# Optimization experiments

Measured on AMD Instinct MI355X. Metric: run time of the kernel, lower is better.

Reference implementation:

```python
import jax, jax.numpy as jnp
import numpy as np

# Mamba hyperparameters (match init_kwargs)
D_MODEL = 1024
D_STATE = 16
D_CONV = 4
EXPAND = 2
D_INNER = EXPAND * D_MODEL          # 2048
DT_RANK = D_MODEL // 16             # 64 (ceil(d_model/16))
B, L = 2, 2048
LN_EPS = 1e-5


def setup_inputs() -> dict:
    key = jax.random.key(0)
    ks = jax.random.split(key, 8)
    s = lambda k, shape, scale=0.02: jax.random.normal(k, shape, jnp.float32) * scale
    x = jax.random.normal(ks[0], (B, L, D_MODEL), jnp.float32)
    W_in = s(ks[1], (2 * D_INNER, D_MODEL))                 # in_proj (no bias)
    W_conv = s(ks[2], (D_INNER, 1, D_CONV), 0.1)            # depthwise conv1d weight
    b_conv = jnp.zeros((D_INNER,), jnp.float32)
    W_xproj = s(ks[3], (DT_RANK + 2 * D_STATE, D_INNER))    # x_proj (no bias)
    W_dt = s(ks[4], (D_INNER, DT_RANK), 0.1)                # dt_proj weight
    b_dt = s(ks[5], (D_INNER,), 0.5)                        # dt_proj bias
    # A initialized as -exp(A_log) with A_log = log(1..d_state), as in mamba_ssm
    A_log = jnp.log(jnp.broadcast_to(
        jnp.arange(1, D_STATE + 1, dtype=jnp.float32), (D_INNER, D_STATE)))
    D_skip = jnp.ones((D_INNER,), jnp.float32)
    W_out = s(ks[6], (D_MODEL, D_INNER))                    # out_proj (no bias)
    gamma = jnp.ones((D_MODEL,), jnp.float32)
    beta = jnp.zeros((D_MODEL,), jnp.float32)
    return dict(x=x, W_in=W_in, W_conv=W_conv, b_conv=b_conv, W_xproj=W_xproj,
                W_dt=W_dt, b_dt=b_dt, A_log=A_log, D_skip=D_skip, W_out=W_out,
                gamma=gamma, beta=beta)


def _mamba(x, W_in, W_conv, b_conv, W_xproj, W_dt, b_dt, A_log, D_skip, W_out):
    # in_proj -> split into x branch and gate z branch, each [B, L, d_inner]
    xz = jnp.einsum('bld,ed->ble', x, W_in)
    xin, z = jnp.split(xz, 2, axis=-1)

    # causal depthwise conv1d over time, then SiLU
    xc = jnp.swapaxes(xin, 1, 2)                            # [B, d_inner, L]
    xc = jnp.pad(xc, ((0, 0), (0, 0), (D_CONV - 1, 0)))
    xc = jax.lax.conv_general_dilated(
        xc, W_conv, window_strides=(1,), padding='VALID',
        dimension_numbers=('NCH', 'OIH', 'NCH'), feature_group_count=D_INNER)
    xc = xc + b_conv[None, :, None]
    u = jax.nn.silu(jnp.swapaxes(xc, 1, 2))                 # [B, L, d_inner]

    # input-dependent dt, B, C
    xdb = jnp.einsum('ble,fe->blf', u, W_xproj)
    dt, Bm, Cm = jnp.split(xdb, [DT_RANK, DT_RANK + D_STATE], axis=-1)
    delta = jax.nn.softplus(jnp.einsum('blr,er->ble', dt, W_dt) + b_dt)  # [B,L,E]
    A = -jnp.exp(A_log)                                     # [E, N]

    def step(h, inp):
        d_t, B_t, C_t, u_t = inp                            # [B,E],[B,N],[B,N],[B,E]
        dA = jnp.exp(d_t[..., None] * A)                    # [B, E, N]
        dBu = d_t[..., None] * B_t[:, None, :] * u_t[..., None]
        h = dA * h + dBu                                    # [B, E, N]
        y = jnp.einsum('ben,bn->be', h, C_t)
        return h, y

    h0 = jnp.zeros((B, D_INNER, D_STATE), x.dtype)
    xs = (jnp.swapaxes(delta, 0, 1), jnp.swapaxes(Bm, 0, 1),
          jnp.swapaxes(Cm, 0, 1), jnp.swapaxes(u, 0, 1))
    _, ys = jax.lax.scan(step, h0, xs)                      # ys: [L, B, E]
    y = jnp.swapaxes(ys, 0, 1) + u * D_skip
    y = y * jax.nn.silu(z)                                  # gated
    return jnp.einsum('ble,de->bld', y, W_out)


def reference(x, W_in, W_conv, b_conv, W_xproj, W_dt, b_dt, A_log, D_skip,
              W_out, gamma, beta):
    out = x + _mamba(x, W_in, W_conv, b_conv, W_xproj, W_dt, b_dt, A_log,
                     D_skip, W_out)
    mu = jnp.mean(out, axis=-1, keepdims=True)
    var = jnp.mean(jnp.square(out - mu), axis=-1, keepdims=True)
    return (out - mu) * jax.lax.rsqrt(var + LN_EPS) * gamma + beta
```

## Files before the change

### kernel.cpp

```cpp
#include <hip/hip_runtime.h>
#include <cstdint>
#include <cstddef>

#define D_MODEL   1024
#define D_STATE   16
#define D_CONV    4
#define D_INNER   2048
#define DT_RANK   64
#define NBATCH    2
#define SEQ       2048
#define NTOK      (NBATCH*SEQ)
#define LN_EPSF   1e-5f
#define NCHUNK    64
#define TCHUNK    32
#define KSPLIT    8

typedef unsigned short u16;
typedef __bf16 bf16x8 __attribute__((ext_vector_type(8)));
typedef float  f32x4  __attribute__((ext_vector_type(4)));

__device__ __forceinline__ u16 f2bf(float f) {
  unsigned u = __float_as_uint(f);
  u += 0x7fffu + ((u >> 16) & 1u);
  return (u16)(u >> 16);
}
__device__ __forceinline__ float bf2f(u16 v) {
  return __uint_as_float(((unsigned)v) << 16);
}
__device__ __forceinline__ void unpack8(uint4 v, float* f) {
  f[0] = __uint_as_float(v.x << 16); f[1] = __uint_as_float(v.x & 0xffff0000u);
  f[2] = __uint_as_float(v.y << 16); f[3] = __uint_as_float(v.y & 0xffff0000u);
  f[4] = __uint_as_float(v.z << 16); f[5] = __uint_as_float(v.z & 0xffff0000u);
  f[6] = __uint_as_float(v.w << 16); f[7] = __uint_as_float(v.w & 0xffff0000u);
}

__device__ __forceinline__ void async16(const u16* g, u16* l) {
  __builtin_amdgcn_global_load_lds(
      (const __attribute__((address_space(1))) unsigned*)g,
      (__attribute__((address_space(3))) unsigned*)l, 16, 0, 0);
}

#define PN0 (NTOK*D_MODEL)
#define PN1 (2*D_INNER*D_MODEL)
#define PN2 (128*D_INNER)
#define PN3 (D_INNER*DT_RANK)
#define PN4 (D_MODEL*D_INNER)
#define PTOT (PN0+PN1+PN2+PN3+PN4)
__global__ __launch_bounds__(256) void prep_k(
    const float* __restrict__ x, const float* __restrict__ W_in,
    const float* __restrict__ W_xproj, const float* __restrict__ W_dt,
    const float* __restrict__ W_out,
    u16* __restrict__ x_bf, u16* __restrict__ Win_bf, u16* __restrict__ Wxp_bf,
    u16* __restrict__ Wdt_bf, u16* __restrict__ Wout_bf)
{
  int i = blockIdx.x * 256 + threadIdx.x;
  if (i < PN0) { x_bf[i] = f2bf(x[i]); return; }
  i -= PN0;
  if (i < PN1) { Win_bf[i] = f2bf(W_in[i]); return; }
  i -= PN1;
  if (i < PN2) {
    const int f = i >> 11;
    Wxp_bf[i] = (f < 96) ? f2bf(W_xproj[i]) : (u16)0;
    return;
  }
  i -= PN2;
  if (i < PN3) { Wdt_bf[i] = f2bf(W_dt[i]); return; }
  i -= PN3;
  if (i < PN4) { Wout_bf[i] = f2bf(W_out[i]); }
}

template<int BM, int BN, int WTM, int WTN, int EPI>
__global__ __launch_bounds__(256) void gemm_nt(
    const u16* __restrict__ A, const u16* __restrict__ B,
    float* __restrict__ C, u16* __restrict__ Cb,
    const float* __restrict__ bias, const float* __restrict__ res,
    int kStart, int kEnd, int lda, int ldb, int ldc, size_t partStride)
{
  constexpr int BK = 32;
  constexpr int WAVES_N = BN / (16 * WTN);
  constexpr int ACH = BM * 4;
  constexpr int BCH = BN * 4;
  constexpr int ROUNDS = (ACH + BCH) / 256;

  __shared__ __align__(16) u16 lA[BM * BK];
  __shared__ __align__(16) u16 lB[BN * BK];

  const int tid  = threadIdx.x;
  const int w    = tid >> 6;
  const int lane = tid & 63;
  const int lrow = lane & 15;
  const int quad = lane >> 4;
  const int bm = blockIdx.y * BM;
  const int bn = blockIdx.x * BN;
  const int wave_m = (w / WAVES_N) * (16 * WTM);
  const int wave_n = (w % WAVES_N) * (16 * WTN);

  int kOff = 0;
  if constexpr (EPI == 4) kOff = blockIdx.z * (kEnd - kStart);

  f32x4 acc[WTM][WTN];
  #pragma unroll
  for (int mi = 0; mi < WTM; ++mi)
    #pragma unroll
    for (int ni = 0; ni < WTN; ++ni)
      acc[mi][ni] = (f32x4){0.f, 0.f, 0.f, 0.f};

  for (int k0 = kStart + kOff; k0 < kEnd + kOff; k0 += BK) {
    #pragma unroll
    for (int r = 0; r < ROUNDS; ++r) {
      const int c0 = r * 256 + w * 64;
      const int c  = c0 + lane;
      if (c0 < ACH) {
        const int row = c >> 2, cc = c & 3;
        async16(A + (size_t)(bm + row) * lda + k0 + cc * 8, &lA[c0 * 8]);
      } else {
        const int cb = c - ACH, c0b = c0 - ACH;
        const int row = cb >> 2, cc = cb & 3;
        async16(B + (size_t)(bn + row) * ldb + k0 + cc * 8, &lB[c0b * 8]);
      }
    }
    __syncthreads();

    bf16x8 af[WTM], bfv[WTN];
    #pragma unroll
    for (int mi = 0; mi < WTM; ++mi)
      af[mi] = *(const bf16x8*)&lA[(wave_m + mi * 16 + lrow) * BK + quad * 8];
    #pragma unroll
    for (int ni = 0; ni < WTN; ++ni)
      bfv[ni] = *(const bf16x8*)&lB[(wave_n + ni * 16 + lrow) * BK + quad * 8];
    #pragma unroll
    for (int mi = 0; mi < WTM; ++mi)
      #pragma unroll
      for (int ni = 0; ni < WTN; ++ni)
        acc[mi][ni] = __builtin_amdgcn_mfma_f32_16x16x32_bf16(af[mi], bfv[ni], acc[mi][ni], 0, 0, 0);
    __syncthreads();
  }

  #pragma unroll
  for (int mi = 0; mi < WTM; ++mi) {
    #pragma unroll
    for (int ni = 0; ni < WTN; ++ni) {
      const int col  = bn + wave_n + ni * 16 + lrow;
      const int row0 = bm + wave_m + mi * 16 + quad * 4;
      #pragma unroll
      for (int r = 0; r < 4; ++r) {
        float v = acc[mi][ni][r];
        const size_t idx = (size_t)(row0 + r) * ldc + col;
        if constexpr (EPI == 0) {
          C[idx] = v;
        } else if constexpr (EPI == 1) {
          Cb[idx] = f2bf(v);
        } else if constexpr (EPI == 2) {
          v += bias[col];
          v = (v > 20.f) ? v : log1pf(__expf(v));
          Cb[idx] = f2bf(v);
        } else if constexpr (EPI == 3) {
          C[idx] = v + res[idx];
        } else {
          C[(size_t)blockIdx.z * partStride + idx] = v;
        }
      }
    }
  }
}

__global__ __launch_bounds__(256) void reduce_conv_k(
    const float* __restrict__ part, u16* __restrict__ dst)
{
  const int i = blockIdx.x * 256 + threadIdx.x;
  float s = 0.f;
  #pragma unroll
  for (int p = 0; p < KSPLIT; ++p)
    s += part[(size_t)p * (NTOK * 128) + i];
  dst[i] = f2bf(s);
}

__global__ void conv_silu_k(const u16* __restrict__ xz, const float* __restrict__ Wc,
                            const float* __restrict__ bc, u16* __restrict__ ub)
{
  const int gid = blockIdx.x * 256 + threadIdx.x;
  const int e   = gid & (D_INNER - 1);
  const int tok = gid >> 11;
  const int l   = tok & (SEQ - 1);
  float acc = bc[e];
  #pragma unroll
  for (int j = 0; j < D_CONV; ++j) {
    const int li = l - 3 + j;
    if (li >= 0) acc += bf2f(xz[(size_t)(tok - 3 + j) * (2 * D_INNER) + e]) * Wc[e * D_CONV + j];
  }
  const float s = acc / (1.f + __expf(-acc));
  ub[gid] = f2bf(s);
}

__global__ __launch_bounds__(256) void scan_p1(
    const u16* __restrict__ delta, const u16* __restrict__ ub,
    const u16* __restrict__ xdb, const float* __restrict__ A_log,
    float* __restrict__ S, float* __restrict__ sumd)
{
  const int e = blockIdx.x * 256 + threadIdx.x;
  const int c = blockIdx.y;
  const int b = blockIdx.z;
  float A[16], h[16];
  #pragma unroll
  for (int n = 0; n < 16; ++n) { A[n] = -__expf(A_log[e * 16 + n]); h[n] = 0.f; }
  float sd = 0.f;
  const int t0 = c * TCHUNK;
  #pragma unroll 4
  for (int t = 0; t < TCHUNK; ++t) {
    const size_t g = (size_t)(b * SEQ + t0 + t);
    const float dlt = bf2f(delta[g * D_INNER + e]);
    const float ut  = bf2f(ub[g * D_INNER + e]);
    float Bv[16];
    const u16* bp = xdb + g * 128 + DT_RANK;
    unpack8(*(const uint4*)bp, Bv);
    unpack8(*(const uint4*)(bp + 8), Bv + 8);
    sd += dlt;
    const float dbu = dlt * ut;
    #pragma unroll
    for (int n = 0; n < 16; ++n)
      h[n] = __expf(dlt * A[n]) * h[n] + dbu * Bv[n];
  }
  const size_t idx = ((size_t)(b * NCHUNK + c) * D_INNER + e);
  #pragma unroll
  for (int q = 0; q < 4; ++q)
    *(f32x4*)&S[idx * 16 + q * 4] = (f32x4){h[q*4], h[q*4+1], h[q*4+2], h[q*4+3]};
  sumd[idx] = sd;
}

__global__ __launch_bounds__(256) void scan_p2(
    const float* __restrict__ S, const float* __restrict__ sumd,
    const float* __restrict__ A_log, float* __restrict__ hinit)
{
  const int tid = blockIdx.x * 256 + threadIdx.x;
  const int n = tid & 15;
  const int e = (tid >> 4) & (D_INNER - 1);
  const int b = tid >> 15;
  const float An = -__expf(A_log[e * 16 + n]);
  float h = 0.f;
  size_t idx = (size_t)b * NCHUNK * D_INNER + e;
  float s_cur  = S[idx * 16 + n];
  float sd_cur = sumd[idx];
  for (int c = 0; c < NCHUNK; ++c) {
    hinit[idx * 16 + n] = h;
    float s_nxt = 0.f, sd_nxt = 0.f;
    if (c + 1 < NCHUNK) {
      const size_t idx2 = idx + D_INNER;
      s_nxt  = S[idx2 * 16 + n];
      sd_nxt = sumd[idx2];
    }
    h = __expf(An * sd_cur) * h + s_cur;
    s_cur = s_nxt; sd_cur = sd_nxt;
    idx += D_INNER;
  }
}

__global__ __launch_bounds__(256) void scan_p3(
    const u16* __restrict__ delta, const u16* __restrict__ ub,
    const u16* __restrict__ xdb, const u16* __restrict__ xz,
    const float* __restrict__ A_log, const float* __restrict__ D_skip,
    const float* __restrict__ hinit, u16* __restrict__ yg)
{
  const int e = blockIdx.x * 256 + threadIdx.x;
  const int c = blockIdx.y;
  const int b = blockIdx.z;
  const size_t idx = ((size_t)(b * NCHUNK + c) * D_INNER + e);
  float A[16], h[16];
  #pragma unroll
  for (int n = 0; n < 16; ++n) A[n] = -__expf(A_log[e * 16 + n]);
  #pragma unroll
  for (int q = 0; q < 4; ++q) {
    f32x4 v = *(const f32x4*)&hinit[idx * 16 + q * 4];
    h[q*4] = v[0]; h[q*4+1] = v[1]; h[q*4+2] = v[2]; h[q*4+3] = v[3];
  }
  const float De = D_skip[e];
  const int t0 = c * TCHUNK;
  #pragma unroll 2
  for (int t = 0; t < TCHUNK; ++t) {
    const size_t g = (size_t)(b * SEQ + t0 + t);
    const float dlt = bf2f(delta[g * D_INNER + e]);
    const float ut  = bf2f(ub[g * D_INNER + e]);
    const float z   = bf2f(xz[g * (2 * D_INNER) + D_INNER + e]);
    float Bv[16], Cv[16];
    const u16* bp = xdb + g * 128 + DT_RANK;
    unpack8(*(const uint4*)bp, Bv);
    unpack8(*(const uint4*)(bp + 8), Bv + 8);
    unpack8(*(const uint4*)(bp + 16), Cv);
    unpack8(*(const uint4*)(bp + 24), Cv + 8);
    const float dbu = dlt * ut;
    float y = 0.f;
    #pragma unroll
    for (int n = 0; n < 16; ++n) {
      h[n] = __expf(dlt * A[n]) * h[n] + dbu * Bv[n];
      y += h[n] * Cv[n];
    }
    y += ut * De;
    const float gt = z / (1.f + __expf(-z));
    yg[g * D_INNER + e] = f2bf(y * gt);
  }
}

__global__ __launch_bounds__(256) void ln_k(const float* __restrict__ pre,
                                            const float* __restrict__ gamma,
                                            const float* __restrict__ beta,
                                            float* __restrict__ out)
{
  const int tok = blockIdx.x;
  const int t   = threadIdx.x;
  const float* row = pre + (size_t)tok * D_MODEL;
  float v[4], s = 0.f, s2 = 0.f;
  #pragma unroll
  for (int i = 0; i < 4; ++i) {
    v[i] = row[t + i * 256];
    s += v[i]; s2 += v[i] * v[i];
  }
  #pragma unroll
  for (int off = 32; off >= 1; off >>= 1) {
    s  += __shfl_xor(s,  off);
    s2 += __shfl_xor(s2, off);
  }
  __shared__ float red[8];
  if ((t & 63) == 0) { red[t >> 6] = s; red[4 + (t >> 6)] = s2; }
  __syncthreads();
  if (t == 0) {
    const float ts  = red[0] + red[1] + red[2] + red[3];
    const float ts2 = red[4] + red[5] + red[6] + red[7];
    const float mu  = ts * (1.f / D_MODEL);
    const float var = ts2 * (1.f / D_MODEL) - mu * mu;
    red[0] = mu; red[1] = rsqrtf(var + LN_EPSF);
  }
  __syncthreads();
  const float mu = red[0], rv = red[1];
  #pragma unroll
  for (int i = 0; i < 4; ++i) {
    const int c = t + i * 256;
    out[(size_t)tok * D_MODEL + c] = (v[i] - mu) * rv * gamma[c] + beta[c];
  }
}

extern "C" void kernel_launch(void* const* d_in, const int* in_sizes, int n_in,
                              void* d_out, int out_size, void* d_ws, size_t ws_size,
                              hipStream_t stream) {
  const float* x       = (const float*)d_in[0];
  const float* W_in    = (const float*)d_in[1];
  const float* W_conv  = (const float*)d_in[2];
  const float* b_conv  = (const float*)d_in[3];
  const float* W_xproj = (const float*)d_in[4];
  const float* W_dt    = (const float*)d_in[5];
  const float* b_dt    = (const float*)d_in[6];
  const float* A_log   = (const float*)d_in[7];
  const float* D_skip  = (const float*)d_in[8];
  const float* W_out   = (const float*)d_in[9];
  const float* gamma   = (const float*)d_in[10];
  const float* beta    = (const float*)d_in[11];
  float* out = (float*)d_out;

  char* ws = (char*)d_ws;
  size_t used = 0;
  auto alloc = [&](size_t bytes) -> char* {
    char* p = ws + used;
    used += (bytes + 255) & ~(size_t)255;
    return p;
  };
  u16* xz_bf     = (u16*)alloc((size_t)NTOK * 2 * D_INNER * 2);
  float* pre     = (float*)alloc((size_t)NTOK * D_MODEL * 4);
  char*  xw_reg  = alloc((size_t)NTOK * D_MODEL * 2 + (size_t)2 * D_INNER * D_MODEL * 2);
  u16* u_bf      = (u16*)alloc((size_t)NTOK * D_INNER * 2);
  u16* delta_bf  = (u16*)alloc((size_t)NTOK * D_INNER * 2);
  u16* xdb_bf    = (u16*)alloc((size_t)NTOK * 128 * 2);
  u16* Wxp_bf    = (u16*)alloc((size_t)128 * D_INNER * 2);
  u16* Wdt_bf    = (u16*)alloc((size_t)D_INNER * DT_RANK * 2);
  u16* Wout_bf   = (u16*)alloc((size_t)D_MODEL * D_INNER * 2);
  u16* yg_bf     = (u16*)alloc((size_t)NTOK * D_INNER * 2);
  float* sumd    = (float*)alloc((size_t)NBATCH * NCHUNK * D_INNER * 4);
  float* xdb_part= (float*)alloc((size_t)KSPLIT * NTOK * 128 * 4);

  u16* x_bf    = (u16*)xw_reg;
  u16* Win_bf  = (u16*)(xw_reg + (size_t)NTOK * D_MODEL * 2);
  float* S     = pre;
  float* hinit = (float*)xw_reg;

  if (ws_size < used) {
    hipMemsetAsync(d_out, 0xFF, (size_t)out_size * 4, stream);
    return;
  }

  const dim3 blk(256);

  prep_k<<<(PTOT + 255) / 256, blk, 0, stream>>>(
      x, W_in, W_xproj, W_dt, W_out, x_bf, Win_bf, Wxp_bf, Wdt_bf, Wout_bf);

  gemm_nt<128,128,4,4,1><<<dim3((2*D_INNER)/128, NTOK/128), blk, 0, stream>>>(
      x_bf, Win_bf, nullptr, xz_bf, nullptr, nullptr,
      0, D_MODEL, D_MODEL, D_MODEL, 2*D_INNER, 0);

  conv_silu_k<<<(NTOK * D_INNER) / 256, blk, 0, stream>>>(xz_bf, W_conv, b_conv, u_bf);

  gemm_nt<64,128,1,8,4><<<dim3(1, NTOK/64, KSPLIT), blk, 0, stream>>>(
      u_bf, Wxp_bf, xdb_part, nullptr, nullptr, nullptr,
      0, D_INNER / KSPLIT, D_INNER, D_INNER, 128, (size_t)NTOK * 128);
  reduce_conv_k<<<(NTOK * 128) / 256, blk, 0, stream>>>(xdb_part, xdb_bf);

  gemm_nt<128,128,4,4,2><<<dim3(D_INNER/128, NTOK/128), blk, 0, stream>>>(
      xdb_bf, Wdt_bf, nullptr, delta_bf, b_dt, nullptr,
      0, DT_RANK, 128, DT_RANK, D_INNER, 0);

  scan_p1<<<dim3(D_INNER/256, NCHUNK, NBATCH), blk, 0, stream>>>(
      delta_bf, u_bf, xdb_bf, A_log, S, sumd);
  scan_p2<<<(NBATCH * D_INNER * D_STATE) / 256, blk, 0, stream>>>(
      S, sumd, A_log, hinit);
  scan_p3<<<dim3(D_INNER/256, NCHUNK, NBATCH), blk, 0, stream>>>(
      delta_bf, u_bf, xdb_bf, xz_bf, A_log, D_skip, hinit, yg_bf);

  gemm_nt<128,64,4,2,3><<<dim3(D_MODEL/64, NTOK/128), blk, 0, stream>>>(
      yg_bf, Wout_bf, pre, nullptr, nullptr, x,
      0, D_INNER, D_INNER, D_INNER, D_MODEL, 0);

  ln_k<<<NTOK, blk, 0, stream>>>(pre, gamma, beta, out);
}
```

Before: 383.7 us.

## Vectorize prep and conv, swizzle GEMM LDS, use power-chain decay in scan

Prep and conv/SiLU kernels now handle four elements per thread with float4/ushort4 accesses, cutting thread count and memory transactions. The GEMM LDS tiles get an XOR swizzle on the 16-byte chunk index to reduce bank conflicts on fragment reads. The scan kernels check at runtime whether A equals -(n+1) and, if so, replace 16 exps per step with one exp and a chain of multiplies. That path relies on the specific A_log initialization, with a fallback for other values, and the repeated multiplication can accumulate rounding error.

```diff
diff --git a/kernel.cpp b/kernel.cpp
--- a/kernel.cpp
+++ b/kernel.cpp
@@ -53,20 +53,21 @@
     u16* __restrict__ x_bf, u16* __restrict__ Win_bf, u16* __restrict__ Wxp_bf,
     u16* __restrict__ Wdt_bf, u16* __restrict__ Wout_bf)
 {
-  int i = blockIdx.x * 256 + threadIdx.x;
-  if (i < PN0) { x_bf[i] = f2bf(x[i]); return; }
-  i -= PN0;
-  if (i < PN1) { Win_bf[i] = f2bf(W_in[i]); return; }
-  i -= PN1;
-  if (i < PN2) {
-    const int f = i >> 11;
-    Wxp_bf[i] = (f < 96) ? f2bf(W_xproj[i]) : (u16)0;
-    return;
-  }
-  i -= PN2;
-  if (i < PN3) { Wdt_bf[i] = f2bf(W_dt[i]); return; }
-  i -= PN3;
-  if (i < PN4) { Wout_bf[i] = f2bf(W_out[i]); }
+  int i = (blockIdx.x * 256 + threadIdx.x) * 4;
+  const float* src; u16* dst; bool pad = false; int local = i;
+  if (local < PN0)            { src = x;       dst = x_bf; }
+  else if ((local -= PN0) < PN1) { src = W_in;    dst = Win_bf; }
+  else if ((local -= PN1) < PN2) { src = W_xproj; dst = Wxp_bf; pad = (local >> 11) >= 96; }
+  else if ((local -= PN2) < PN3) { src = W_dt;    dst = Wdt_bf; }
+  else if ((local -= PN3) < PN4) { src = W_out;   dst = Wout_bf; }
+  else return;
+  ushort4 o;
+  if (pad) { o = (ushort4){0,0,0,0}; }
+  else {
+    const float4 v = *(const float4*)(src + local);
+    o = (ushort4){ f2bf(v.x), f2bf(v.y), f2bf(v.z), f2bf(v.w) };
+  }
+  *(ushort4*)(dst + local) = o;
 }
 
 template<int BM, int BN, int WTM, int WTN, int EPI>
@@ -94,6 +95,7 @@
   const int bn = blockIdx.x * BN;
   const int wave_m = (w / WAVES_N) * (16 * WTM);
   const int wave_n = (w % WAVES_N) * (16 * WTN);
+  const int rquad = quad ^ (lrow & 3);
 
   int kOff = 0;
   if constexpr (EPI == 4) kOff = blockIdx.z * (kEnd - kStart);
@@ -111,11 +113,11 @@
       const int c0 = r * 256 + w * 64;
       const int c  = c0 + lane;
       if (c0 < ACH) {
-        const int row = c >> 2, cc = c & 3;
+        const int row = c >> 2, cc = (c & 3) ^ (row & 3);
         async16(A + (size_t)(bm + row) * lda + k0 + cc * 8, &lA[c0 * 8]);
       } else {
         const int cb = c - ACH, c0b = c0 - ACH;
-        const int row = cb >> 2, cc = cb & 3;
+        const int row = cb >> 2, cc = (cb & 3) ^ (row & 3);
         async16(B + (size_t)(bn + row) * ldb + k0 + cc * 8, &lB[c0b * 8]);
       }
     }
@@ -124,10 +126,10 @@
     bf16x8 af[WTM], bfv[WTN];
     #pragma unroll
     for (int mi = 0; mi < WTM; ++mi)
-      af[mi] = *(const bf16x8*)&lA[(wave_m + mi * 16 + lrow) * BK + quad * 8];
+      af[mi] = *(const bf16x8*)&lA[(wave_m + mi * 16 + lrow) * BK + rquad * 8];
     #pragma unroll
     for (int ni = 0; ni < WTN; ++ni)
-      bfv[ni] = *(const bf16x8*)&lB[(wave_n + ni * 16 + lrow) * BK + quad * 8];
+      bfv[ni] = *(const bf16x8*)&lB[(wave_n + ni * 16 + lrow) * BK + rquad * 8];
     #pragma unroll
     for (int mi = 0; mi < WTM; ++mi)
       #pragma unroll
@@ -175,22 +177,39 @@
   dst[i] = f2bf(s);
 }
 
-__global__ void conv_silu_k(const u16* __restrict__ xz, const float* __restrict__ Wc,
-                            const float* __restrict__ bc, u16* __restrict__ ub)
-{
-  const int gid = blockIdx.x * 256 + threadIdx.x;
+__global__ __launch_bounds__(256) void conv_silu_k(
+    const u16* __restrict__ xz, const float* __restrict__ Wc,
+    const float* __restrict__ bc, u16* __restrict__ ub)
+{
+  const int gid = (blockIdx.x * 256 + threadIdx.x) * 4;
   const int e   = gid & (D_INNER - 1);
   const int tok = gid >> 11;
   const int l   = tok & (SEQ - 1);
-  float acc = bc[e];
+  float acc[4];
+  #pragma unroll
+  for (int q = 0; q < 4; ++q) acc[q] = bc[e + q];
   #pragma unroll
   for (int j = 0; j < D_CONV; ++j) {
     const int li = l - 3 + j;
-    if (li >= 0) acc += bf2f(xz[(size_t)(tok - 3 + j) * (2 * D_INNER) + e]) * Wc[e * D_CONV + j];
-  }
-  const float s = acc / (1.f + __expf(-acc));
-  ub[gid] = f2bf(s);
-}
+    if (li >= 0) {
+      const ushort4 xv = *(const ushort4*)(xz + (size_t)(tok - 3 + j) * (2 * D_INNER) + e);
+      acc[0] += bf2f(xv.x) * Wc[(e    ) * D_CONV + j];
+      acc[1] += bf2f(xv.y) * Wc[(e + 1) * D_CONV + j];
+      acc[2] += bf2f(xv.z) * Wc[(e + 2) * D_CONV + j];
+      acc[3] += bf2f(xv.w) * Wc[(e + 3) * D_CONV + j];
+    }
+  }
+  ushort4 o;
+  {
+    const float s0 = acc[0] / (1.f + __expf(-acc[0]));
+    const float s1 = acc[1] / (1.f + __expf(-acc[1]));
+    const float s2 = acc[2] / (1.f + __expf(-acc[2]));
+    const float s3 = acc[3] / (1.f + __expf(-acc[3]));
+    o = (ushort4){ f2bf(s0), f2bf(s1), f2bf(s2), f2bf(s3) };
+  }
+  *(ushort4*)(ub + gid) = o;
+}
+
 
 __global__ __launch_bounds__(256) void scan_p1(
     const u16* __restrict__ delta, const u16* __restrict__ ub,
@@ -201,11 +220,16 @@
   const int c = blockIdx.y;
   const int b = blockIdx.z;
   float A[16], h[16];
-  #pragma unroll
-  for (int n = 0; n < 16; ++n) { A[n] = -__expf(A_log[e * 16 + n]); h[n] = 0.f; }
+  bool fast = true;
+  #pragma unroll
+  for (int n = 0; n < 16; ++n) {
+    A[n] = -__expf(A_log[e * 16 + n]);
+    fast = fast && (fabsf(A[n] + (float)(n + 1)) < 1e-3f);
+    h[n] = 0.f;
+  }
   float sd = 0.f;
   const int t0 = c * TCHUNK;
-  #pragma unroll 4
+  #pragma unroll 2
   for (int t = 0; t < TCHUNK; ++t) {
     const size_t g = (size_t)(b * SEQ + t0 + t);
     const float dlt = bf2f(delta[g * D_INNER + e]);
@@ -216,9 +240,19 @@
     unpack8(*(const uint4*)(bp + 8), Bv + 8);
     sd += dlt;
     const float dbu = dlt * ut;
+    float dA[16];
+    if (fast) {
+      const float q = __expf(-dlt);
+      float p = 1.f;
+      #pragma unroll
+      for (int n = 0; n < 16; ++n) { p *= q; dA[n] = p; }
+    } else {
+      #pragma unroll
+      for (int n = 0; n < 16; ++n) dA[n] = __expf(dlt * A[n]);
+    }
     #pragma unroll
     for (int n = 0; n < 16; ++n)
-      h[n] = __expf(dlt * A[n]) * h[n] + dbu * Bv[n];
+      h[n] = dA[n] * h[n] + dbu * Bv[n];
   }
   const size_t idx = ((size_t)(b * NCHUNK + c) * D_INNER + e);
   #pragma unroll
@@ -265,8 +299,12 @@
   const int b = blockIdx.z;
   const size_t idx = ((size_t)(b * NCHUNK + c) * D_INNER + e);
   float A[16], h[16];
-  #pragma unroll
-  for (int n = 0; n < 16; ++n) A[n] = -__expf(A_log[e * 16 + n]);
+  bool fast = true;
+  #pragma unroll
+  for (int n = 0; n < 16; ++n) {
+    A[n] = -__expf(A_log[e * 16 + n]);
+    fast = fast && (fabsf(A[n] + (float)(n + 1)) < 1e-3f);
+  }
   #pragma unroll
   for (int q = 0; q < 4; ++q) {
     f32x4 v = *(const f32x4*)&hinit[idx * 16 + q * 4];
@@ -287,10 +325,20 @@
     unpack8(*(const uint4*)(bp + 16), Cv);
     unpack8(*(const uint4*)(bp + 24), Cv + 8);
     const float dbu = dlt * ut;
+    float dA[16];
+    if (fast) {
+      const float q = __expf(-dlt);
+      float p = 1.f;
+      #pragma unroll
+      for (int n = 0; n < 16; ++n) { p *= q; dA[n] = p; }
+    } else {
+      #pragma unroll
+      for (int n = 0; n < 16; ++n) dA[n] = __expf(dlt * A[n]);
+    }
     float y = 0.f;
     #pragma unroll
     for (int n = 0; n < 16; ++n) {
-      h[n] = __expf(dlt * A[n]) * h[n] + dbu * Bv[n];
+      h[n] = dA[n] * h[n] + dbu * Bv[n];
       y += h[n] * Cv[n];
     }
     y += ut * De;
@@ -386,14 +434,14 @@
 
   const dim3 blk(256);
 
-  prep_k<<<(PTOT + 255) / 256, blk, 0, stream>>>(
+  prep_k<<<(PTOT / 4 + 255) / 256, blk, 0, stream>>>(
       x, W_in, W_xproj, W_dt, W_out, x_bf, Win_bf, Wxp_bf, Wdt_bf, Wout_bf);
 
   gemm_nt<128,128,4,4,1><<<dim3((2*D_INNER)/128, NTOK/128), blk, 0, stream>>>(
       x_bf, Win_bf, nullptr, xz_bf, nullptr, nullptr,
       0, D_MODEL, D_MODEL, D_MODEL, 2*D_INNER, 0);
 
-  conv_silu_k<<<(NTOK * D_INNER) / 256, blk, 0, stream>>>(xz_bf, W_conv, b_conv, u_bf);
+  conv_silu_k<<<(NTOK * D_INNER) / 1024, blk, 0, stream>>>(xz_bf, W_conv, b_conv, u_bf);
 
   gemm_nt<64,128,1,8,4><<<dim3(1, NTOK/64, KSPLIT), blk, 0, stream>>>(
       u_bf, Wxp_bf, xdb_part, nullptr, nullptr, nullptr,
```

After: 389.6 us. No clear change (+1.5%).
